# Optimization experiments

Measured on AMD Instinct MI355X. Metric: run time of the kernel, lower is better.

Reference implementation:

```python
import jax, jax.numpy as jnp
import numpy as np

EPS = 1e-05
N = 8192


def setup_inputs() -> dict:
    key = jax.random.key(0)
    k1, k2 = jax.random.split(key)
    params = jax.random.normal(k1, (3,), dtype=jnp.float32) * 0.1
    # sparse-ish symmetric 0/1 adjacency, float32 like the torch buffer
    a = (jax.random.uniform(k2, (N, N)) < 0.005).astype(jnp.float32)
    graph = jnp.maximum(a, a.T)
    return {"params": params, "graph": graph}


def reference(params, graph):
    alpha, beta, sigma = params[0], params[1], params[2]
    n = graph.shape[0]
    # p == 0 => sum_degrees(v) is just the degree (row sum) of v
    deg = jnp.sum(graph, axis=1)                       # [n]
    s = alpha * deg[:, None] + beta * deg[None, :] + sigma   # [n, n]
    p = 1.0 / (1.0 + jnp.exp(s))                        # logistic prob
    ll = jnp.where(graph == 1.0,
                   jnp.log(p + EPS),
                   jnp.log(1.0 - p + EPS))
    # loop runs over i <= j: upper triangle including diagonal
    upper = jnp.triu(jnp.ones((n, n), dtype=bool))
    likelihood = jnp.sum(jnp.where(upper, ll, 0.0))
    return -likelihood
```

## Files before the change

kernel.cpp:

```cpp
#include <hip/hip_runtime.h>

#define N 8192
#define EPS 1e-5f
#define LOG2E 1.4426950408889634f
#define LN2d  0.6931471805599453

#define TR 64
#define TC 256
#define NBJ 32
#define NBI 128
#define RPW 16
#define CAPW 512
#define SEG_W 4096
#define NTILES 2112
#define NSEG (NTILES * 4)
#define NDENSE 4096
#define NFB 1024
#define TBLMAX 1024

static const size_t OFF_ACC = 0;
static const size_t OFF_DEG = 4096;
static const size_t OFF_CNT = OFF_DEG + (size_t)N * 4;
static const size_t OFF_EDG = OFF_CNT + (size_t)NSEG * 4;
static const size_t WS_NEED = OFF_EDG + (size_t)NSEG * SEG_W * 4;

__device__ __forceinline__ unsigned mbcnt64(unsigned long long m) {
    return __builtin_amdgcn_mbcnt_hi((unsigned)(m >> 32),
           __builtin_amdgcn_mbcnt_lo((unsigned)m, 0u));
}

__global__ __launch_bounds__(256) void k_pass1(const float* __restrict__ g,
        float* __restrict__ deg, unsigned* __restrict__ cnt,
        unsigned* __restrict__ edges, const int segmode) {
    const int bj = (int)blockIdx.x & (NBJ - 1);
    const int bi = (int)blockIdx.x >> 5;
    if (bi > 4 * bj + 3) return;
    const int r0 = bi * TR, c0 = bj * TC;
    const int wave = threadIdx.x >> 6, lane = threadIdx.x & 63;
    const int aid = 2 * bj * (bj + 1) + bi;

    __shared__ float    scol[TC];
    __shared__ unsigned buf[4][CAPW];
    scol[threadIdx.x] = 0.f;
    __syncthreads();

    const int c = c0 + lane * 4;
    const int rbase = r0 + wave * RPW;
    const float* __restrict__ gp = g + (size_t)rbase * N + c;
    unsigned* __restrict__ myseg = edges + ((size_t)aid * 4 + wave) * SEG_W;
    unsigned wc = 0, wflushed = 0;
    float ca0 = 0.f, ca1 = 0.f, ca2 = 0.f, ca3 = 0.f;

#define EMIT(BB, PRED, OFFv) \
    if (BB) { if (segmode && (PRED)) buf[wave][wc + mbcnt64(BB)] = etag | (OFFv); \
        const unsigned p_ = __popcll(BB); wc += p_; rsum += p_; }

#define FLUSHCHK \
    if (segmode && wc > (unsigned)(CAPW - 256)) { \
        for (unsigned t_ = lane; t_ < wc; t_ += 64) myseg[wflushed + t_] = buf[wave][t_]; \
        wflushed += wc; wc = 0; }

    if (r0 + TR <= c0) {
        #pragma unroll 4
        for (int k = 0; k < RPW; ++k) {
            const float4 v = *reinterpret_cast<const float4*>(gp + (size_t)k * N);
            FLUSHCHK
            ca0 += v.x; ca1 += v.y; ca2 += v.z; ca3 += v.w;
            const unsigned long long b0 = __ballot(v.x != 0.f);
            const unsigned long long b1 = __ballot(v.y != 0.f);
            const unsigned long long b2 = __ballot(v.z != 0.f);
            const unsigned long long b3 = __ballot(v.w != 0.f);
            if (b0 | b1 | b2 | b3) {
                const int gr = rbase + k;
                const unsigned etag = ((unsigned)gr << 16) | (unsigned)c;
                unsigned rsum = 0;
                EMIT(b0, v.x != 0.f, 0u)
                EMIT(b1, v.y != 0.f, 1u)
                EMIT(b2, v.z != 0.f, 2u)
                EMIT(b3, v.w != 0.f, 3u)
                if (lane == 0) atomicAdd(&deg[gr], (float)rsum);
            }
        }
    } else {
        for (int k = 0; k < RPW; ++k) {
            const int gr = rbase + k;
            const float4 v = *reinterpret_cast<const float4*>(gp + (size_t)k * N);
            FLUSHCHK
            const bool a0 = (v.x != 0.f) && (c + 0 >= gr);
            const bool a1 = (v.y != 0.f) && (c + 1 >= gr);
            const bool a2 = (v.z != 0.f) && (c + 2 >= gr);
            const bool a3 = (v.w != 0.f) && (c + 3 >= gr);
            ca0 += (c + 0 > gr) ? v.x : 0.f;
            ca1 += (c + 1 > gr) ? v.y : 0.f;
            ca2 += (c + 2 > gr) ? v.z : 0.f;
            ca3 += (c + 3 > gr) ? v.w : 0.f;
            const unsigned long long b0 = __ballot(a0);
            const unsigned long long b1 = __ballot(a1);
            const unsigned long long b2 = __ballot(a2);
            const unsigned long long b3 = __ballot(a3);
            if (b0 | b1 | b2 | b3) {
                const unsigned etag = ((unsigned)gr << 16) | (unsigned)c;
                unsigned rsum = 0;
                EMIT(b0, a0, 0u)
                EMIT(b1, a1, 1u)
                EMIT(b2, a2, 2u)
                EMIT(b3, a3, 3u)
                if (lane == 0) atomicAdd(&deg[gr], (float)rsum);
            }
        }
    }
#undef EMIT
#undef FLUSHCHK

    if (segmode) {
        for (unsigned t = lane; t < wc; t += 64) myseg[wflushed + t] = buf[wave][t];
        if (lane == 0) cnt[aid * 4 + wave] = wflushed + wc;
    }
    if (ca0 != 0.f) atomicAdd(&scol[lane * 4 + 0], ca0);
    if (ca1 != 0.f) atomicAdd(&scol[lane * 4 + 1], ca1);
    if (ca2 != 0.f) atomicAdd(&scol[lane * 4 + 2], ca2);
    if (ca3 != 0.f) atomicAdd(&scol[lane * 4 + 3], ca3);
    __syncthreads();
    const float sv = scol[threadIdx.x];
    if (sv != 0.f) atomicAdd(&deg[c0 + threadIdx.x], sv);
}

__global__ __launch_bounds__(256) void k_ll(const float* __restrict__ g,
        const float* __restrict__ deg, const float* __restrict__ params,
        const unsigned* __restrict__ cnt, const unsigned* __restrict__ edges,
        double* __restrict__ accv, const int segmode) {
    __shared__ float  tbl[2][TBLMAX];
    __shared__ double wsum[4];
    __shared__ float  rmn[4], rmx[4];
    const int tid = threadIdx.x;
    const int wv = tid >> 6, ln = tid & 63;
    const int b = blockIdx.x;
    const float alpha = params[0], beta = params[1], sigma = params[2];
    double dlocal = 0.0;

    if (b < NDENSE) {
        if (!segmode) return;
        const int r1 = b, r2 = N - 1 - b;
        const float b2 = beta * LOG2E;
        const float base1 = fmaf(alpha, deg[r1], sigma) * LOG2E;
        const float base2 = fmaf(alpha, deg[r2], sigma) * LOG2E;

        float mn = 3.0e38f, mx = -3.0e38f;
        for (int j = r1 + tid; j < N; j += 256) {
            const float d = deg[j];
            mn = fminf(mn, d); mx = fmaxf(mx, d);
        }
        #pragma unroll
        for (int off = 32; off; off >>= 1) {
            mn = fminf(mn, __shfl_xor(mn, off));
            mx = fmaxf(mx, __shfl_xor(mx, off));
        }
        if (ln == 0) { rmn[wv] = mn; rmx[wv] = mx; }
        __syncthreads();
        mn = fminf(fminf(rmn[0], rmn[1]), fminf(rmn[2], rmn[3]));
        mx = fmaxf(fmaxf(rmx[0], rmx[1]), fmaxf(rmx[2], rmx[3]));
        const int dmin = (int)mn;
        const int R = (int)mx - dmin + 1;

#define DEVAL(DV, BASE) \
        __builtin_amdgcn_logf(1.00001f - __builtin_amdgcn_rcpf(1.f + \
            __builtin_amdgcn_exp2f(fmaf(b2, (DV), (BASE)))))

        float l0 = 0.f, l1 = 0.f, l2 = 0.f, l3 = 0.f;
        if (R <= TBLMAX) {
            for (int i = tid; i < R; i += 256) {
                const float dv = (float)(dmin + i);
                tbl[0][i] = DEVAL(dv, base1);
                tbl[1][i] = DEVAL(dv, base2);
            }
            __syncthreads();
            int j = r1 + tid;
            for (; j + 768 < N; j += 1024) {
                l0 += tbl[0][(int)deg[j]       - dmin];
                l1 += tbl[0][(int)deg[j + 256] - dmin];
                l2 += tbl[0][(int)deg[j + 512] - dmin];
                l3 += tbl[0][(int)deg[j + 768] - dmin];
            }
            for (; j < N; j += 256) l0 += tbl[0][(int)deg[j] - dmin];
            j = r2 + tid;
            for (; j + 768 < N; j += 1024) {
                l0 += tbl[1][(int)deg[j]       - dmin];
                l1 += tbl[1][(int)deg[j + 256] - dmin];
                l2 += tbl[1][(int)deg[j + 512] - dmin];
                l3 += tbl[1][(int)deg[j + 768] - dmin];
            }
            for (; j < N; j += 256) l0 += tbl[1][(int)deg[j] - dmin];
        } else {
            int j = r1 + tid;
            for (; j + 768 < N; j += 1024) {
                l0 += DEVAL(deg[j], base1);
                l1 += DEVAL(deg[j + 256], base1);
                l2 += DEVAL(deg[j + 512], base1);
                l3 += DEVAL(deg[j + 768], base1);
            }
            for (; j < N; j += 256) l0 += DEVAL(deg[j], base1);
            j = r2 + tid;
            for (; j + 768 < N; j += 1024) {
                l0 += DEVAL(deg[j], base2);
                l1 += DEVAL(deg[j + 256], base2);
                l2 += DEVAL(deg[j + 512], base2);
                l3 += DEVAL(deg[j + 768], base2);
            }
            for (; j < N; j += 256) l0 += DEVAL(deg[j], base2);
        }
#undef DEVAL
        dlocal = (double)((l0 + l1) + (l2 + l3)) * LN2d;
    } else if (b < NDENSE + NTILES) {
        if (!segmode) return;
        const int aid = b - NDENSE;
        float local = 0.f;
        for (int w = 0; w < 4; ++w) {
            const unsigned n = cnt[aid * 4 + w];
            const unsigned* __restrict__ seg = edges + ((size_t)aid * 4 + w) * SEG_W;
            for (unsigned t = tid; t < n; t += 256) {
                const unsigned e = seg[t];
                const float di = deg[e >> 16];
                const float dj = deg[e & 0xffffu];
                const float s = fmaf(alpha, di, fmaf(beta, dj, sigma));
                const float p = __fdividef(1.f, 1.f + __expf(s));
                local += __logf(p + EPS) - __logf(1.f - p + EPS);
            }
        }
        dlocal = (double)local;
    } else {
        if (segmode) return;
        const int rb = b - NDENSE - NTILES;
        for (int q = 0; q < 8; ++q) {
            const int i = rb * 8 + q;
            const float base = fmaf(alpha, deg[i], sigma);
            float rl = 0.f;
            for (int j = i + tid; j < N; j += 256) {
                const float s = fmaf(beta, deg[j], base);
                const float p = __fdividef(1.f, 1.f + __expf(s));
                const float gv = g[(size_t)i * N + j];
                rl += (gv != 0.f) ? __logf(p + EPS) : __logf(1.f - p + EPS);
            }
            dlocal += (double)rl;
        }
    }

    #pragma unroll
    for (int off = 32; off; off >>= 1) dlocal += __shfl_xor(dlocal, off);
    if (ln == 0) wsum[wv] = dlocal;
    __syncthreads();
    if (tid == 0) {
        const double t = (wsum[0] + wsum[1]) + (wsum[2] + wsum[3]);
        if (t != 0.0) atomicAdd(&accv[(b & 63) * 8], t);
    }
}

__global__ void k_final(const double* __restrict__ accv, float* __restrict__ out) {
    double v = accv[threadIdx.x * 8];
    #pragma unroll
    for (int off = 32; off; off >>= 1) v += __shfl_xor(v, off);
    if (threadIdx.x == 0) out[0] = (float)(-v);
}

extern "C" void kernel_launch(void* const* d_in, const int* in_sizes, int n_in,
                              void* d_out, int out_size, void* d_ws, size_t ws_size,
                              hipStream_t stream) {
    const float* params = (const float*)d_in[0];
    const float* graph  = (const float*)d_in[1];
    float* out = (float*)d_out;

    char* ws = (char*)d_ws;
    double*   accv  = (double*)(ws + OFF_ACC);
    float*    deg   = (float*)(ws + OFF_DEG);
    unsigned* cnt   = (unsigned*)(ws + OFF_CNT);
    unsigned* edges = (unsigned*)(ws + OFF_EDG);
    const int segmode = (ws_size >= WS_NEED) ? 1 : 0;

    hipMemsetAsync(ws, 0, OFF_DEG + (size_t)N * 4, stream);
    k_pass1<<<NBI * NBJ, 256, 0, stream>>>(graph, deg, cnt, edges, segmode);
    const int llgrid = segmode ? (NDENSE + NTILES) : (NDENSE + NTILES + NFB);
    k_ll<<<llgrid, 256, 0, stream>>>(graph, deg, params, cnt, edges, accv, segmode);
    k_final<<<1, 64, 0, stream>>>(accv, out);
}
```

Baseline: 66.59 us.

## Replace dense upper-triangle sum with degree-histogram symmetric decomposition

The dense no-edge term over the upper triangle is now computed algebraically. The full R×R sum over the degree histogram, plus the diagonal, is halved. An antisymmetric correction block adds the difference between the (i,j) and (j,i) orientations using prefix histograms over 32 chunks of 256 columns. This replaces 4096 blocks that each looped over a row with about 33 blocks whose work scales with the number of distinct degree values. A per-row fallback covers wide degree ranges. The correction blocks run serial per-thread loops and double accumulation, which could become a latency tail.

```diff
diff --git a/kernel.cpp b/kernel.cpp
--- a/kernel.cpp
+++ b/kernel.cpp
@@ -14,9 +14,11 @@
 #define SEG_W 4096
 #define NTILES 2112
 #define NSEG (NTILES * 4)
-#define NDENSE 4096
+#define RMAX 512
+#define NA 32
+#define NDR 1024
+#define EDGE0 (NA + 1 + NDR)
 #define NFB 1024
-#define TBLMAX 1024
 
 static const size_t OFF_ACC = 0;
 static const size_t OFF_DEG = 4096;
@@ -129,90 +131,101 @@
         const float* __restrict__ deg, const float* __restrict__ params,
         const unsigned* __restrict__ cnt, const unsigned* __restrict__ edges,
         double* __restrict__ accv, const int segmode) {
-    __shared__ float  tbl[2][TBLMAX];
     __shared__ double wsum[4];
-    __shared__ float  rmn[4], rmx[4];
+    __shared__ float  srange[8];
+    __shared__ int    hist[RMAX];
+    __shared__ float  dchunk[256];
     const int tid = threadIdx.x;
     const int wv = tid >> 6, ln = tid & 63;
     const int b = blockIdx.x;
     const float alpha = params[0], beta = params[1], sigma = params[2];
+    const float a2 = alpha * LOG2E, b2 = beta * LOG2E, s2 = sigma * LOG2E;
     double dlocal = 0.0;
 
-    if (b < NDENSE) {
+#define F2(X, Y) __builtin_amdgcn_logf(1.00001f - __builtin_amdgcn_rcpf(1.f + \
+        __builtin_amdgcn_exp2f(fmaf(a2, (X), fmaf(b2, (Y), s2)))))
+
+    if (b < EDGE0) {
+        if (segmode) {
+            float mn = 3.0e38f, mx = -3.0e38f;
+            for (int j = tid; j < N; j += 256) {
+                const float d = deg[j];
+                mn = fminf(mn, d); mx = fmaxf(mx, d);
+            }
+            #pragma unroll
+            for (int off = 32; off; off >>= 1) {
+                mn = fminf(mn, __shfl_xor(mn, off));
+                mx = fmaxf(mx, __shfl_xor(mx, off));
+            }
+            if (ln == 0) { srange[wv] = mn; srange[4 + wv] = mx; }
+            __syncthreads();
+            mn = fminf(fminf(srange[0], srange[1]), fminf(srange[2], srange[3]));
+            mx = fmaxf(fmaxf(srange[4], srange[5]), fmaxf(srange[6], srange[7]));
+            const int dmin = (int)mn;
+            const int R = (int)mx - dmin + 1;
+
+            if (b < NA) {
+                if (R <= RMAX) {
+                    const int j0 = b * 256;
+                    for (int i = tid; i < R; i += 256) hist[i] = 0;
+                    __syncthreads();
+                    for (int i = tid; i < j0; i += 256)
+                        atomicAdd(&hist[(int)deg[i] - dmin], 1);
+                    dchunk[tid] = deg[j0 + tid];
+                    __syncthreads();
+                    const float dj = dchunk[tid];
+                    double accA = 0.0;
+                    for (int i = 0; i < tid; ++i) {
+                        const float di = dchunk[i];
+                        accA += (double)(F2(di, dj) - F2(dj, di));
+                    }
+                    for (int d = 0; d < R; ++d) {
+                        const int c = hist[d];
+                        if (c) {
+                            const float dd = (float)(dmin + d);
+                            accA += (double)c * (double)(F2(dd, dj) - F2(dj, dd));
+                        }
+                    }
+                    dlocal = accA * 0.5 * LN2d;
+                }
+            } else if (b == NA) {
+                if (R <= RMAX) {
+                    for (int i = tid; i < R; i += 256) hist[i] = 0;
+                    __syncthreads();
+                    for (int i = tid; i < N; i += 256)
+                        atomicAdd(&hist[(int)deg[i] - dmin], 1);
+                    __syncthreads();
+                    double accT = 0.0;
+                    const int RR = R * R;
+                    for (int cell = tid; cell < RR; cell += 256) {
+                        const int a = cell / R, bb = cell - a * R;
+                        const long long c = (long long)hist[a] * hist[bb];
+                        if (c) accT += (double)c *
+                            (double)F2((float)(dmin + a), (float)(dmin + bb));
+                    }
+                    for (int a = tid; a < R; a += 256) {
+                        if (hist[a]) accT += (double)hist[a] *
+                            (double)F2((float)(dmin + a), (float)(dmin + a));
+                    }
+                    dlocal = accT * 0.5 * LN2d;
+                }
+            } else {
+                if (R > RMAX) {
+                    const int db = b - NA - 1;
+                    float ls = 0.f;
+                    for (int q = 0; q < 4; ++q) {
+                        const int r1 = db + q * NDR, r2 = N - 1 - r1;
+                        const float dr1 = deg[r1], dr2 = deg[r2];
+                        for (int j = r1 + tid; j < N; j += 256) ls += F2(dr1, deg[j]);
+                        for (int j = r2 + tid; j < N; j += 256) ls += F2(dr2, deg[j]);
+                    }
+                    dlocal = (double)ls * LN2d;
+                }
+            }
+        }
+    } else if (b < EDGE0 + NTILES) {
         if (!segmode) return;
-        const int r1 = b, r2 = N - 1 - b;
-        const float b2 = beta * LOG2E;
-        const float base1 = fmaf(alpha, deg[r1], sigma) * LOG2E;
-        const float base2 = fmaf(alpha, deg[r2], sigma) * LOG2E;
-
-        float mn = 3.0e38f, mx = -3.0e38f;
-        for (int j = r1 + tid; j < N; j += 256) {
-            const float d = deg[j];
-            mn = fminf(mn, d); mx = fmaxf(mx, d);
-        }
-        #pragma unroll
-        for (int off = 32; off; off >>= 1) {
-            mn = fminf(mn, __shfl_xor(mn, off));
-            mx = fmaxf(mx, __shfl_xor(mx, off));
-        }
-        if (ln == 0) { rmn[wv] = mn; rmx[wv] = mx; }
-        __syncthreads();
-        mn = fminf(fminf(rmn[0], rmn[1]), fminf(rmn[2], rmn[3]));
-        mx = fmaxf(fmaxf(rmx[0], rmx[1]), fmaxf(rmx[2], rmx[3]));
-        const int dmin = (int)mn;
-        const int R = (int)mx - dmin + 1;
-
-#define DEVAL(DV, BASE) \
-        __builtin_amdgcn_logf(1.00001f - __builtin_amdgcn_rcpf(1.f + \
-            __builtin_amdgcn_exp2f(fmaf(b2, (DV), (BASE)))))
-
-        float l0 = 0.f, l1 = 0.f, l2 = 0.f, l3 = 0.f;
-        if (R <= TBLMAX) {
-            for (int i = tid; i < R; i += 256) {
-                const float dv = (float)(dmin + i);
-                tbl[0][i] = DEVAL(dv, base1);
-                tbl[1][i] = DEVAL(dv, base2);
-            }
-            __syncthreads();
-            int j = r1 + tid;
-            for (; j + 768 < N; j += 1024) {
-                l0 += tbl[0][(int)deg[j]       - dmin];
-                l1 += tbl[0][(int)deg[j + 256] - dmin];
-                l2 += tbl[0][(int)deg[j + 512] - dmin];
-                l3 += tbl[0][(int)deg[j + 768] - dmin];
-            }
-            for (; j < N; j += 256) l0 += tbl[0][(int)deg[j] - dmin];
-            j = r2 + tid;
-            for (; j + 768 < N; j += 1024) {
-                l0 += tbl[1][(int)deg[j]       - dmin];
-                l1 += tbl[1][(int)deg[j + 256] - dmin];
-                l2 += tbl[1][(int)deg[j + 512] - dmin];
-                l3 += tbl[1][(int)deg[j + 768] - dmin];
-            }
-            for (; j < N; j += 256) l0 += tbl[1][(int)deg[j] - dmin];
-        } else {
-            int j = r1 + tid;
-            for (; j + 768 < N; j += 1024) {
-                l0 += DEVAL(deg[j], base1);
-                l1 += DEVAL(deg[j + 256], base1);
-                l2 += DEVAL(deg[j + 512], base1);
-                l3 += DEVAL(deg[j + 768], base1);
-            }
-            for (; j < N; j += 256) l0 += DEVAL(deg[j], base1);
-            j = r2 + tid;
-            for (; j + 768 < N; j += 1024) {
-                l0 += DEVAL(deg[j], base2);
-                l1 += DEVAL(deg[j + 256], base2);
-                l2 += DEVAL(deg[j + 512], base2);
-                l3 += DEVAL(deg[j + 768], base2);
-            }
-            for (; j < N; j += 256) l0 += DEVAL(deg[j], base2);
-        }
-#undef DEVAL
-        dlocal = (double)((l0 + l1) + (l2 + l3)) * LN2d;
-    } else if (b < NDENSE + NTILES) {
-        if (!segmode) return;
-        const int aid = b - NDENSE;
+        const int aid = b - EDGE0;
         float local = 0.f;
         for (int w = 0; w < 4; ++w) {
             const unsigned n = cnt[aid * 4 + w];
@@ -229,7 +242,7 @@
         dlocal = (double)local;
     } else {
         if (segmode) return;
-        const int rb = b - NDENSE - NTILES;
+        const int rb = b - EDGE0 - NTILES;
         for (int q = 0; q < 8; ++q) {
             const int i = rb * 8 + q;
             const float base = fmaf(alpha, deg[i], sigma);
@@ -243,6 +256,7 @@
             dlocal += (double)rl;
         }
     }
+#undef F2
 
     #pragma unroll
     for (int off = 32; off; off >>= 1) dlocal += __shfl_xor(dlocal, off);
@@ -277,7 +291,7 @@
 
     hipMemsetAsync(ws, 0, OFF_DEG + (size_t)N * 4, stream);
     k_pass1<<<NBI * NBJ, 256, 0, stream>>>(graph, deg, cnt, edges, segmode);
-    const int llgrid = segmode ? (NDENSE + NTILES) : (NDENSE + NTILES + NFB);
+    const int llgrid = segmode ? (EDGE0 + NTILES) : (EDGE0 + NTILES + NFB);
     k_ll<<<llgrid, 256, 0, stream>>>(graph, deg, params, cnt, edges, accv, segmode);
     k_final<<<1, 64, 0, stream>>>(accv, out);
 }
```

New measurement: 72.43 us. +8.8%, slower.
